# Kernel optimization log

Hardware: AMD Instinct MI355X
Metric: run time of the kernel (lower is better)

The kernel has to match this reference:

```python
import jax, jax.numpy as jnp
import numpy as np

B, T, HID = 2, 2048, 2048
NH, NKV, D = 16, 4, 128
WIN = 512
ROPE_BASE = 10000.0
SCALE = D ** -0.5
EPS = 1e-12


def setup_inputs() -> dict:
    key = jax.random.key(0)
    ks = jax.random.split(key, 5)
    x = jax.random.normal(ks[0], (B, T, HID), dtype=jnp.float32)
    wq = jax.random.normal(ks[1], (HID, NH * D), dtype=jnp.float32) * 0.02
    wk = jax.random.normal(ks[2], (HID, NKV * D), dtype=jnp.float32) * 0.02
    wv = jax.random.normal(ks[3], (HID, NKV * D), dtype=jnp.float32) * 0.02
    wo = jax.random.normal(ks[4], (NH * D, HID), dtype=jnp.float32) * 0.02
    return {"x": x, "wq": wq, "wk": wk, "wv": wv, "wo": wo}


def _rope_tables(t, offset=0):
    inv_freq = 1.0 / (ROPE_BASE ** (jnp.arange(0, D, 2, dtype=jnp.float32) / D))
    pos = jnp.arange(offset, offset + t, dtype=jnp.float32)
    freqs = pos[:, None] * inv_freq[None, :]              # [t, D/2]
    cos = jnp.concatenate([jnp.cos(freqs), jnp.cos(freqs)], axis=-1)  # [t, D]
    sin = jnp.concatenate([jnp.sin(freqs), jnp.sin(freqs)], axis=-1)
    return cos, sin


def _apply_rope(x, cos, sin):
    # x: [B, H, T, D]; rotate-half formulation
    x1, x2 = jnp.split(x, 2, axis=-1)
    rot = jnp.concatenate([-x2, x1], axis=-1)
    return x * cos[None, None] + rot * sin[None, None]


def _l2norm(x):
    n = jnp.sqrt(jnp.sum(x * x, axis=-1, keepdims=True))
    return x / jnp.maximum(n, EPS)


def _forward(x, wq, wk, wv, wo):
    b, t, _ = x.shape
    q = (x @ wq).reshape(b, t, NH, D).transpose(0, 2, 1, 3)    # [B,H,T,D]
    k = (x @ wk).reshape(b, t, NKV, D).transpose(0, 2, 1, 3)   # [B,Hk,T,D]
    v = (x @ wv).reshape(b, t, NKV, D).transpose(0, 2, 1, 3)
    q = _l2norm(q)
    k = _l2norm(k)
    cos, sin = _rope_tables(t, offset=0)
    q = _apply_rope(q, cos, sin)
    k = _apply_rope(k, cos, sin)
    rep = NH // NKV
    k = jnp.repeat(k, rep, axis=1)                             # GQA repeat_interleave
    v = jnp.repeat(v, rep, axis=1)
    i = jnp.arange(t)
    allowed = (i[None, :] <= i[:, None]) & (i[None, :] > i[:, None] - WIN)  # [T,T]
    logits = jnp.einsum("bhid,bhjd->bhij", q, k) * SCALE
    logits = jnp.where(allowed[None, None], logits, -jnp.inf)
    attn = jax.nn.softmax(logits, axis=-1)
    out = jnp.einsum("bhij,bhjd->bhid", attn, v)
    out = out.transpose(0, 2, 1, 3).reshape(b, t, NH * D)
    return out @ wo


def reference(x, wq, wk, wv, wo):
    return _forward(x, wq, wk, wv, wo)
```

## Files before the change

kernel.cpp:

```cpp
#include <hip/hip_runtime.h>
#include <hip/hip_bf16.h>
#include <cstdint>

#define NHQ 16
#define NKVH 4
#define HDIM 128
#define WINSZ 512
#define TSEQ 2048
#define ATTN_SCALE 0.08838834764831845f

typedef __attribute__((ext_vector_type(8))) short s16x8;
typedef __attribute__((ext_vector_type(4))) float f32x4;

__device__ __forceinline__ void gload16(const void* g, void* lds) {
  __builtin_amdgcn_global_load_lds(
      (const __attribute__((address_space(1))) unsigned int*)g,
      (__attribute__((address_space(3))) unsigned int*)(uintptr_t)lds,
      16, 0, 0);
}

__device__ __forceinline__ f32x4 mfma16(s16x8 a, s16x8 b, f32x4 c) {
  return __builtin_amdgcn_mfma_f32_16x16x32_bf16(a, b, c, 0, 0, 0);
}

#define SBAR() asm volatile("s_barrier" ::: "memory")
#define VMCNT(n) asm volatile("s_waitcnt vmcnt(" #n ")" ::: "memory")
#define LGKM(n) asm volatile("s_waitcnt lgkmcnt(" #n ")" ::: "memory")

__global__ __launch_bounds__(256) void rope_tables_kernel(float* __restrict__ cosT,
                                                          float* __restrict__ sinT) {
  int idx = blockIdx.x * 256 + threadIdx.x;
  int t = idx >> 6, d2 = idx & 63;
  float inv = powf(10000.0f, -(float)d2 / 64.0f);
  float a = (float)t * inv;
  cosT[idx] = cosf(a);
  sinT[idx] = sinf(a);
}

__global__ __launch_bounds__(256) void cast_kernel(const float* __restrict__ in,
                                                   __bf16* __restrict__ out, int n4) {
  int i = blockIdx.x * 256 + threadIdx.x;
  if (i >= n4) return;
  float4 v = ((const float4*)in)[i];
  union { __bf16 h[4]; uint2 u; } pk;
  pk.h[0] = (__bf16)v.x; pk.h[1] = (__bf16)v.y; pk.h[2] = (__bf16)v.z; pk.h[3] = (__bf16)v.w;
  ((uint2*)out)[i] = pk.u;
}

__global__ __launch_bounds__(256) void transpose_cast(const float* __restrict__ in,
                                                      __bf16* __restrict__ out, int R, int C) {
  __shared__ float tile[32][33];
  int c0 = blockIdx.x * 32, r0 = blockIdx.y * 32;
  int tx = threadIdx.x, ty = threadIdx.y;
#pragma unroll
  for (int i = 0; i < 4; i++)
    tile[ty + i * 8][tx] = in[(size_t)(r0 + ty + i * 8) * C + c0 + tx];
  __syncthreads();
#pragma unroll
  for (int i = 0; i < 4; i++)
    out[(size_t)(c0 + ty + i * 8) * R + r0 + tx] = (__bf16)tile[tx][ty + i * 8];
}

template <int MODE>
__global__ __launch_bounds__(512, 2) void gemm8(const __bf16* __restrict__ A,
                                                const __bf16* __restrict__ Bt,
                                                float* __restrict__ Cf,
                                                __bf16* __restrict__ Qo, __bf16* __restrict__ Ko,
                                                __bf16* __restrict__ Vo, int M, int N, int K) {
  __shared__ __attribute__((aligned(16))) char Lds[2][65536];

  const int tid = threadIdx.x;
  const int w = tid >> 6, lane = tid & 63;
  const int wm = w >> 2, wn = w & 3;

  const int nbx = gridDim.x;
  const int nwg = nbx * gridDim.y;
  const int bid = blockIdx.y * nbx + blockIdx.x;
  const int q8 = nwg >> 3, r8 = nwg & 7;
  const int xcd = bid & 7, idx = bid >> 3;
  const int swz = (xcd < r8 ? xcd * (q8 + 1) : r8 * (q8 + 1) + (xcd - r8) * q8) + idx;
  const int bx = swz % nbx, by = swz / nbx;
  const int m0 = by * 256, n0 = bx * 256;

  const int ru = tid >> 3;
  const int cs = (tid & 7) ^ (ru & 7);
  const __bf16* gAs = A + (size_t)(m0 + ru) * K + cs * 8;
  const __bf16* gBs = Bt + (size_t)(n0 + ru) * K + cs * 8;

  auto stA = [&](int tt, int u) {
    gload16(gAs + (size_t)(64 * u) * K + tt * 64, Lds[tt & 1] + u * 8192 + w * 1024);
  };
  auto stB = [&](int tt, int u) {
    gload16(gBs + (size_t)(64 * u) * K + tt * 64, Lds[tt & 1] + 32768 + u * 8192 + w * 1024);
  };

  const int rowb = (lane & 15) * 128;
  const int cph0 = (((lane >> 4)) ^ (lane & 7)) * 16;
  const int cph1 = ((4 + (lane >> 4)) ^ (lane & 7)) * 16;
  const int Abase = wm * 16384;
  const int Bbase = 32768 + wn * 8192;

  f32x4 acc[8][4];
  f32x4 zero = {0.f, 0.f, 0.f, 0.f};
#pragma unroll
  for (int i = 0; i < 8; i++)
#pragma unroll
    for (int j = 0; j < 4; j++) acc[i][j] = zero;

  const int NT = K >> 6;

#pragma unroll
  for (int u = 0; u < 4; u++) stA(0, u);
#pragma unroll
  for (int u = 0; u < 4; u++) stB(0, u);
#pragma unroll
  for (int u = 0; u < 4; u++) stA(1, u);
#pragma unroll
  for (int u = 0; u < 4; u++) stB(1, u);
  VMCNT(8);
  SBAR();

  s16x8 fa[4][2], fb[4][2];

  for (int t = 0; t < NT; ++t) {
    const char* bs = Lds[t & 1];
    const bool more = (t + 2) < NT;

#pragma unroll
    for (int mi = 0; mi < 4; mi++) {
      fa[mi][0] = *(const s16x8*)(bs + Abase + mi * 2048 + rowb + cph0);
      fa[mi][1] = *(const s16x8*)(bs + Abase + mi * 2048 + rowb + cph1);
    }
#pragma unroll
    for (int ni = 0; ni < 2; ni++) {
      fb[ni][0] = *(const s16x8*)(bs + Bbase + ni * 2048 + rowb + cph0);
      fb[ni][1] = *(const s16x8*)(bs + Bbase + ni * 2048 + rowb + cph1);
    }
    SBAR();
    LGKM(0);
    __builtin_amdgcn_sched_barrier(0);
    __builtin_amdgcn_s_setprio(1);
#pragma unroll
    for (int mi = 0; mi < 4; mi++)
#pragma unroll
      for (int ni = 0; ni < 2; ni++)
#pragma unroll
        for (int kk = 0; kk < 2; kk++)
          acc[mi][ni] = mfma16(fa[mi][kk], fb[ni][kk], acc[mi][ni]);
    __builtin_amdgcn_s_setprio(0);
    SBAR();

#pragma unroll
    for (int ni = 2; ni < 4; ni++) {
      fb[ni][0] = *(const s16x8*)(bs + Bbase + ni * 2048 + rowb + cph0);
      fb[ni][1] = *(const s16x8*)(bs + Bbase + ni * 2048 + rowb + cph1);
    }
    if (more) { stA(t + 2, 0); stA(t + 2, 2); }
    SBAR();
    LGKM(0);
    __builtin_amdgcn_sched_barrier(0);
    __builtin_amdgcn_s_setprio(1);
#pragma unroll
    for (int mi = 0; mi < 4; mi++)
#pragma unroll
      for (int ni = 2; ni < 4; ni++)
#pragma unroll
        for (int kk = 0; kk < 2; kk++)
          acc[mi][ni] = mfma16(fa[mi][kk], fb[ni][kk], acc[mi][ni]);
    __builtin_amdgcn_s_setprio(0);
    SBAR();

#pragma unroll
    for (int mi = 0; mi < 4; mi++) {
      fa[mi][0] = *(const s16x8*)(bs + Abase + 8192 + mi * 2048 + rowb + cph0);
      fa[mi][1] = *(const s16x8*)(bs + Abase + 8192 + mi * 2048 + rowb + cph1);
    }
    if (more) { stB(t + 2, 0); stB(t + 2, 1); stB(t + 2, 2); stB(t + 2, 3); }
    SBAR();
    LGKM(0);
    __builtin_amdgcn_sched_barrier(0);
    __builtin_amdgcn_s_setprio(1);
#pragma unroll
    for (int mi = 0; mi < 4; mi++)
#pragma unroll
      for (int ni = 0; ni < 2; ni++)
#pragma unroll
        for (int kk = 0; kk < 2; kk++)
          acc[4 + mi][ni] = mfma16(fa[mi][kk], fb[ni][kk], acc[4 + mi][ni]);
    __builtin_amdgcn_s_setprio(0);
    SBAR();

    if (more) { stA(t + 2, 1); stA(t + 2, 3); }
    if (t + 2 < NT) {
      VMCNT(8);
    } else if (t + 1 < NT) {
      VMCNT(0);
    }
    SBAR();
    __builtin_amdgcn_s_setprio(1);
#pragma unroll
    for (int mi = 0; mi < 4; mi++)
#pragma unroll
      for (int ni = 2; ni < 4; ni++)
#pragma unroll
        for (int kk = 0; kk < 2; kk++)
          acc[4 + mi][ni] = mfma16(fa[mi][kk], fb[ni][kk], acc[4 + mi][ni]);
    __builtin_amdgcn_s_setprio(0);
    SBAR();
  }

#pragma unroll
  for (int mf = 0; mf < 8; mf++)
#pragma unroll
    for (int nf = 0; nf < 4; nf++) {
      int rbase = m0 + wm * 128 + mf * 16 + (lane >> 4) * 4;
      int col = n0 + wn * 64 + nf * 16 + (lane & 15);
#pragma unroll
      for (int r = 0; r < 4; r++) {
        int m = rbase + r;
        float v = acc[mf][nf][r];
        if constexpr (MODE == 0) {
          Cf[(size_t)m * N + col] = v;
        } else {
          int b = m >> 11, tq = m & 2047;
          __bf16 bv = (__bf16)v;
          if (col < 2048) {
            Qo[(((size_t)(b * NHQ + (col >> 7))) * TSEQ + tq) * HDIM + (col & 127)] = bv;
          } else if (col < 2560) {
            int c2 = col - 2048;
            Ko[(((size_t)(b * NKVH + (c2 >> 7))) * TSEQ + tq) * HDIM + (c2 & 127)] = bv;
          } else {
            int c2 = col - 2560;
            Vo[(((size_t)(b * NKVH + (c2 >> 7))) * TSEQ + tq) * HDIM + (c2 & 127)] = bv;
          }
        }
      }
    }
}

__global__ __launch_bounds__(256) void normrope(__bf16* __restrict__ Q, __bf16* __restrict__ Kk,
                                                const float* __restrict__ cosT,
                                                const float* __restrict__ sinT) {
  int w = threadIdx.x >> 6, lane = threadIdx.x & 63;
  int row = blockIdx.x / 5;
  int slot = (blockIdx.x % 5) * 4 + w;
  int b = row >> 11, t = row & 2047;
  __bf16* p;
  if (slot < 16)
    p = Q + (((size_t)(b * NHQ + slot)) * TSEQ + t) * HDIM;
  else
    p = Kk + (((size_t)(b * NKVH + (slot - 16))) * TSEQ + t) * HDIM;
  float x1 = (float)p[lane], x2 = (float)p[lane + 64];
  float ss = x1 * x1 + x2 * x2;
#pragma unroll
  for (int off = 32; off; off >>= 1) ss += __shfl_xor(ss, off);
  float inv = 1.0f / fmaxf(sqrtf(ss), 1e-12f);
  x1 *= inv;
  x2 *= inv;
  float c = cosT[t * 64 + lane], s = sinT[t * 64 + lane];
  p[lane] = (__bf16)(x1 * c - x2 * s);
  p[lane + 64] = (__bf16)(x2 * c + x1 * s);
}

__global__ __launch_bounds__(256) void attn_kernel(const __bf16* __restrict__ Qf,
                                                   const __bf16* __restrict__ Kf,
                                                   const __bf16* __restrict__ Vf,
                                                   __bf16* __restrict__ Ab) {
  __shared__ __align__(16) __bf16 Kl[32 * 136];
  __shared__ __align__(16) __bf16 Vt[128 * 40];
  __shared__ __align__(16) __bf16 Pl[4][16 * 40];
  int tid = threadIdx.x, w = tid >> 6, lane = tid & 63;
  int bid = blockIdx.x;
  int qt = bid & 31, h = (bid >> 5) & 15, b = bid >> 9;
  int qs = qt * 64;
  int kvh = h >> 2;
  const __bf16* Qb = Qf + ((size_t)(b * NHQ + h) * TSEQ) * HDIM;
  const __bf16* Kb = Kf + ((size_t)(b * NKVH + kvh) * TSEQ) * HDIM;
  const __bf16* Vb = Vf + ((size_t)(b * NKVH + kvh) * TSEQ) * HDIM;

  s16x8 aq[4];
  int qrow_f = qs + w * 16 + (lane & 15);
#pragma unroll
  for (int kb = 0; kb < 4; kb++)
    aq[kb] = *(const s16x8*)(Qb + (size_t)qrow_f * HDIM + kb * 32 + (lane >> 4) * 8);

  f32x4 acc[8];
  f32x4 zero = {0.f, 0.f, 0.f, 0.f};
#pragma unroll
  for (int db = 0; db < 8; db++) acc[db] = zero;
  float mrow[4], lrow[4];
#pragma unroll
  for (int r = 0; r < 4; r++) { mrow[r] = -1e30f; lrow[r] = 0.f; }

  int lo = qs - (WINSZ - 1);
  if (lo < 0) lo = 0;
  lo &= ~31;

  for (int ks = lo; ks <= qs + 63; ks += 32) {
    __syncthreads();
#pragma unroll
    for (int i = 0; i < 2; i++) {
      int c = tid + 256 * i;
      int j = c >> 4, dk = (c & 15) * 8;
      int4 kv = *(const int4*)(Kb + (size_t)(ks + j) * HDIM + dk);
      *(int4*)&Kl[j * 136 + dk] = kv;
      int jv = c & 31, d0 = (c >> 5) * 8;
      int4 vv = *(const int4*)(Vb + (size_t)(ks + jv) * HDIM + d0);
      const __bf16* pv = (const __bf16*)&vv;
#pragma unroll
      for (int e = 0; e < 8; e++) Vt[(d0 + e) * 40 + jv] = pv[e];
    }
    __syncthreads();

    f32x4 sacc[2];
    sacc[0] = zero; sacc[1] = zero;
#pragma unroll
    for (int jb = 0; jb < 2; jb++)
#pragma unroll
      for (int kb = 0; kb < 4; kb++) {
        s16x8 bk = *(const s16x8*)&Kl[(jb * 16 + (lane & 15)) * 136 + kb * 32 + (lane >> 4) * 8];
        sacc[jb] = mfma16(aq[kb], bk, sacc[jb]);
      }

    int colbase = ks + (lane & 15);
    float p0v[4], p1v[4], scf[4];
#pragma unroll
    for (int r = 0; r < 4; r++) {
      int qrow = qs + w * 16 + (lane >> 4) * 4 + r;
      float s0 = sacc[0][r] * ATTN_SCALE, s1 = sacc[1][r] * ATTN_SCALE;
      int j0 = colbase, j1 = colbase + 16;
      bool a0 = (j0 <= qrow) && (j0 > qrow - WINSZ);
      bool a1 = (j1 <= qrow) && (j1 > qrow - WINSZ);
      float mt = fmaxf(a0 ? s0 : -1e30f, a1 ? s1 : -1e30f);
#pragma unroll
      for (int off = 1; off < 16; off <<= 1) mt = fmaxf(mt, __shfl_xor(mt, off));
      float mn = fmaxf(mrow[r], mt);
      float p0 = a0 ? __expf(s0 - mn) : 0.f;
      float p1 = a1 ? __expf(s1 - mn) : 0.f;
      float sf = __expf(mrow[r] - mn);
      float ts = p0 + p1;
#pragma unroll
      for (int off = 1; off < 16; off <<= 1) ts += __shfl_xor(ts, off);
      lrow[r] = lrow[r] * sf + ts;
      mrow[r] = mn;
      p0v[r] = p0; p1v[r] = p1; scf[r] = sf;
    }

#pragma unroll
    for (int r = 0; r < 4; r++) {
      Pl[w][((lane >> 4) * 4 + r) * 40 + 0 * 16 + (lane & 15)] = (__bf16)p0v[r];
      Pl[w][((lane >> 4) * 4 + r) * 40 + 1 * 16 + (lane & 15)] = (__bf16)p1v[r];
    }
#pragma unroll
    for (int db = 0; db < 8; db++) {
      f32x4 t = acc[db];
#pragma unroll
      for (int r = 0; r < 4; r++) t[r] *= scf[r];
      acc[db] = t;
    }

    s16x8 pa = *(const s16x8*)&Pl[w][(lane & 15) * 40 + (lane >> 4) * 8];
#pragma unroll
    for (int db = 0; db < 8; db++) {
      s16x8 bv = *(const s16x8*)&Vt[(db * 16 + (lane & 15)) * 40 + (lane >> 4) * 8];
      acc[db] = mfma16(pa, bv, acc[db]);
    }
  }

#pragma unroll
  for (int db = 0; db < 8; db++)
#pragma unroll
    for (int r = 0; r < 4; r++) {
      int qrow = qs + w * 16 + (lane >> 4) * 4 + r;
      float v = acc[db][r] / lrow[r];
      Ab[((size_t)(b * TSEQ + qrow)) * 2048 + h * HDIM + db * 16 + (lane & 15)] = (__bf16)v;
    }
}

extern "C" void kernel_launch(void* const* d_in, const int* in_sizes, int n_in,
                              void* d_out, int out_size, void* d_ws, size_t ws_size,
                              hipStream_t stream) {
  const float* x = (const float*)d_in[0];
  const float* wq = (const float*)d_in[1];
  const float* wk = (const float*)d_in[2];
  const float* wv = (const float*)d_in[3];
  const float* wo = (const float*)d_in[4];
  float* out = (float*)d_out;

  char* ws = (char*)d_ws;
  size_t off = 0;
  auto alloc = [&](size_t bytes) -> void* {
    void* p = ws + off;
    off += (bytes + 255) & ~(size_t)255;
    return p;
  };
  __bf16* Xb = (__bf16*)alloc((size_t)4096 * 2048 * 2);
  __bf16* Wqkvt = (__bf16*)alloc((size_t)3072 * 2048 * 2);
  __bf16* Wot = (__bf16*)alloc((size_t)2048 * 2048 * 2);
  __bf16* Q = (__bf16*)alloc((size_t)2 * NHQ * TSEQ * HDIM * 2);
  __bf16* Kb = (__bf16*)alloc((size_t)2 * NKVH * TSEQ * HDIM * 2);
  __bf16* Vb = (__bf16*)alloc((size_t)2 * NKVH * TSEQ * HDIM * 2);
  float* cosT = (float*)alloc((size_t)TSEQ * 64 * 4);
  float* sinT = (float*)alloc((size_t)TSEQ * 64 * 4);
  __bf16* Ab = Xb;

  rope_tables_kernel<<<TSEQ * 64 / 256, 256, 0, stream>>>(cosT, sinT);
  cast_kernel<<<8192, 256, 0, stream>>>(x, Xb, 2097152);
  dim3 tb(32, 8);
  transpose_cast<<<dim3(64, 64), tb, 0, stream>>>(wq, Wqkvt, 2048, 2048);
  transpose_cast<<<dim3(16, 64), tb, 0, stream>>>(wk, Wqkvt + (size_t)2048 * 2048, 2048, 512);
  transpose_cast<<<dim3(16, 64), tb, 0, stream>>>(wv, Wqkvt + (size_t)2560 * 2048, 2048, 512);
  transpose_cast<<<dim3(64, 64), tb, 0, stream>>>(wo, Wot, 2048, 2048);

  gemm8<1><<<dim3(12, 16), 512, 0, stream>>>(Xb, Wqkvt, nullptr, Q, Kb, Vb, 4096, 3072, 2048);
  normrope<<<4096 * 5, 256, 0, stream>>>(Q, Kb, cosT, sinT);
  attn_kernel<<<2 * NHQ * (TSEQ / 64), 256, 0, stream>>>(Q, Kb, Vb, Ab);
  gemm8<0><<<dim3(8, 16), 512, 0, stream>>>(Ab, Wot, out, nullptr, nullptr, nullptr, 4096, 2048,
                                            2048);
}
```

Measured before the change: 233.2 us.

## Pre-transpose V and software-pipeline attention with 64-key tiles and swizzled LDS

```diff
diff --git a/kernel.cpp b/kernel.cpp
--- a/kernel.cpp
+++ b/kernel.cpp
@@ -59,6 +59,23 @@
 #pragma unroll
   for (int i = 0; i < 4; i++)
     out[(size_t)(c0 + ty + i * 8) * R + r0 + tx] = (__bf16)tile[tx][ty + i * 8];
+}
+
+__global__ __launch_bounds__(256) void vtrans(const __bf16* __restrict__ V,
+                                              __bf16* __restrict__ VT) {
+  __shared__ __bf16 t32[32][33];
+  int bh = blockIdx.z;
+  int t0 = blockIdx.y * 32, d0 = blockIdx.x * 32;
+  const __bf16* src = V + (size_t)bh * TSEQ * HDIM;
+  __bf16* dst = VT + (size_t)bh * HDIM * TSEQ;
+  int tx = threadIdx.x, ty = threadIdx.y;
+#pragma unroll
+  for (int i = 0; i < 4; i++)
+    t32[ty + i * 8][tx] = src[(size_t)(t0 + ty + i * 8) * HDIM + d0 + tx];
+  __syncthreads();
+#pragma unroll
+  for (int i = 0; i < 4; i++)
+    dst[(size_t)(d0 + ty + i * 8) * TSEQ + t0 + tx] = t32[tx][ty + i * 8];
 }
 
 template <int MODE>
@@ -264,11 +281,11 @@
 
 __global__ __launch_bounds__(256) void attn_kernel(const __bf16* __restrict__ Qf,
                                                    const __bf16* __restrict__ Kf,
-                                                   const __bf16* __restrict__ Vf,
+                                                   const __bf16* __restrict__ VTf,
                                                    __bf16* __restrict__ Ab) {
-  __shared__ __align__(16) __bf16 Kl[32 * 136];
-  __shared__ __align__(16) __bf16 Vt[128 * 40];
-  __shared__ __align__(16) __bf16 Pl[4][16 * 40];
+  __shared__ __attribute__((aligned(16))) char KlB[64 * 256];
+  __shared__ __attribute__((aligned(16))) char VtB[128 * 128];
+  __shared__ __attribute__((aligned(16))) char PlB[4 * 2048];
   int tid = threadIdx.x, w = tid >> 6, lane = tid & 63;
   int bid = blockIdx.x;
   int qt = bid & 31, h = (bid >> 5) & 15, b = bid >> 9;
@@ -276,7 +293,8 @@
   int kvh = h >> 2;
   const __bf16* Qb = Qf + ((size_t)(b * NHQ + h) * TSEQ) * HDIM;
   const __bf16* Kb = Kf + ((size_t)(b * NKVH + kvh) * TSEQ) * HDIM;
-  const __bf16* Vb = Vf + ((size_t)(b * NKVH + kvh) * TSEQ) * HDIM;
+  const __bf16* VTb = VTf + ((size_t)(b * NKVH + kvh) * HDIM) * TSEQ;
+  char* Pw = PlB + w * 2048;
 
   s16x8 aq[4];
   int qrow_f = qs + w * 16 + (lane & 15);
@@ -294,78 +312,117 @@
 
   int lo = qs - (WINSZ - 1);
   if (lo < 0) lo = 0;
-  lo &= ~31;
-
-  for (int ks = lo; ks <= qs + 63; ks += 32) {
+  lo &= ~63;
+  const int nt = ((qs + 64) - lo) >> 6;
+
+  int4 kE[4], vE[4], kO[4], vO[4];
+
+#define ATTN_LOAD(KR, VR, KS)                                                      \
+  _Pragma("unroll") for (int i = 0; i < 4; i++) {                                  \
+    KR[i] = *(const int4*)(Kb + (size_t)((KS) + (tid >> 4) + 16 * i) * HDIM +      \
+                           (tid & 15) * 8);                                        \
+    VR[i] = *(const int4*)(VTb + (size_t)((tid >> 3) + 32 * i) * TSEQ + (KS) +     \
+                           (tid & 7) * 8);                                         \
+  }
+
+#define ATTN_WRITE(KR, VR)                                                         \
+  _Pragma("unroll") for (int i = 0; i < 4; i++) {                                  \
+    int jrow = (tid >> 4) + 16 * i;                                                \
+    *(int4*)(KlB + jrow * 256 + (((tid & 15) * 16) ^ ((jrow & 7) << 4))) = KR[i];  \
+    int drow = (tid >> 3) + 32 * i;                                                \
+    *(int4*)(VtB + drow * 128 + (((tid & 7) * 16) ^ ((drow & 7) << 4))) = VR[i];   \
+  }
+
+#define ATTN_COMPUTE(KS)                                                           \
+  {                                                                                \
+    f32x4 sacc[4];                                                                 \
+    _Pragma("unroll") for (int jb = 0; jb < 4; jb++) sacc[jb] = zero;              \
+    _Pragma("unroll") for (int jb = 0; jb < 4; jb++) {                             \
+      int key = jb * 16 + (lane & 15);                                             \
+      _Pragma("unroll") for (int kb = 0; kb < 4; kb++) {                           \
+        s16x8 bk = *(const s16x8*)(KlB + key * 256 +                               \
+                                   ((kb * 64 + (lane >> 4) * 16) ^ ((key & 7) << 4))); \
+        sacc[jb] = mfma16(aq[kb], bk, sacc[jb]);                                   \
+      }                                                                            \
+    }                                                                              \
+    float scf[4];                                                                  \
+    _Pragma("unroll") for (int r = 0; r < 4; r++) {                                \
+      int qrow = qs + w * 16 + (lane >> 4) * 4 + r;                                \
+      float sv[4]; bool av[4];                                                     \
+      _Pragma("unroll") for (int jb = 0; jb < 4; jb++) {                           \
+        int j = (KS) + jb * 16 + (lane & 15);                                      \
+        av[jb] = (j <= qrow) && (j > qrow - WINSZ);                                \
+        sv[jb] = sacc[jb][r] * ATTN_SCALE;                                         \
+      }                                                                            \
+      float mt = -1e30f;                                                           \
+      _Pragma("unroll") for (int jb = 0; jb < 4; jb++)                             \
+        mt = fmaxf(mt, av[jb] ? sv[jb] : -1e30f);                                  \
+      _Pragma("unroll") for (int off = 1; off < 16; off <<= 1)                     \
+        mt = fmaxf(mt, __shfl_xor(mt, off));                                       \
+      float mn = fmaxf(mrow[r], mt);                                               \
+      float pv_[4]; float ts = 0.f;                                                \
+      _Pragma("unroll") for (int jb = 0; jb < 4; jb++) {                           \
+        pv_[jb] = av[jb] ? __expf(sv[jb] - mn) : 0.f;                              \
+        ts += pv_[jb];                                                             \
+      }                                                                            \
+      _Pragma("unroll") for (int off = 1; off < 16; off <<= 1)                     \
+        ts += __shfl_xor(ts, off);                                                 \
+      float sf = __expf(mrow[r] - mn);                                             \
+      lrow[r] = lrow[r] * sf + ts;                                                 \
+      mrow[r] = mn;                                                                \
+      scf[r] = sf;                                                                 \
+      int q = (lane >> 4) * 4 + r;                                                 \
+      _Pragma("unroll") for (int jb = 0; jb < 4; jb++)                             \
+        *(__bf16*)(Pw + q * 128 +                                                  \
+                   (((jb * 16 + (lane & 15)) * 2) ^ ((q & 7) << 4))) = (__bf16)pv_[jb]; \
+    }                                                                              \
+    _Pragma("unroll") for (int db = 0; db < 8; db++) {                             \
+      f32x4 tt = acc[db];                                                          \
+      _Pragma("unroll") for (int r = 0; r < 4; r++) tt[r] *= scf[r];               \
+      acc[db] = tt;                                                                \
+    }                                                                              \
+    s16x8 pa[2];                                                                   \
+    _Pragma("unroll") for (int kb = 0; kb < 2; kb++) {                             \
+      int q = lane & 15;                                                           \
+      pa[kb] = *(const s16x8*)(Pw + q * 128 +                                      \
+                               ((kb * 64 + (lane >> 4) * 16) ^ ((q & 7) << 4)));   \
+    }                                                                              \
+    _Pragma("unroll") for (int db = 0; db < 8; db++) {                             \
+      int d = db * 16 + (lane & 15);                                               \
+      _Pragma("unroll") for (int kb = 0; kb < 2; kb++) {                           \
+        s16x8 bv = *(const s16x8*)(VtB + d * 128 +                                 \
+                                   ((kb * 64 + (lane >> 4) * 16) ^ ((d & 7) << 4))); \
+        acc[db] = mfma16(pa[kb], bv, acc[db]);                                     \
+      }                                                                            \
+    }                                                                              \
+  }
+
+  int ks = lo;
+  ATTN_LOAD(kE, vE, ks);
+  int it = 0;
+  for (; it + 2 <= nt; it += 2) {
+    ATTN_WRITE(kE, vE);
+    ATTN_LOAD(kO, vO, ks + 64);
     __syncthreads();
-#pragma unroll
-    for (int i = 0; i < 2; i++) {
-      int c = tid + 256 * i;
-      int j = c >> 4, dk = (c & 15) * 8;
-      int4 kv = *(const int4*)(Kb + (size_t)(ks + j) * HDIM + dk);
-      *(int4*)&Kl[j * 136 + dk] = kv;
-      int jv = c & 31, d0 = (c >> 5) * 8;
-      int4 vv = *(const int4*)(Vb + (size_t)(ks + jv) * HDIM + d0);
-      const __bf16* pv = (const __bf16*)&vv;
-#pragma unroll
-      for (int e = 0; e < 8; e++) Vt[(d0 + e) * 40 + jv] = pv[e];
-    }
+    ATTN_COMPUTE(ks);
     __syncthreads();
-
-    f32x4 sacc[2];
-    sacc[0] = zero; sacc[1] = zero;
-#pragma unroll
-    for (int jb = 0; jb < 2; jb++)
-#pragma unroll
-      for (int kb = 0; kb < 4; kb++) {
-        s16x8 bk = *(const s16x8*)&Kl[(jb * 16 + (lane & 15)) * 136 + kb * 32 + (lane >> 4) * 8];
-        sacc[jb] = mfma16(aq[kb], bk, sacc[jb]);
-      }
-
-    int colbase = ks + (lane & 15);
-    float p0v[4], p1v[4], scf[4];
-#pragma unroll
-    for (int r = 0; r < 4; r++) {
-      int qrow = qs + w * 16 + (lane >> 4) * 4 + r;
-      float s0 = sacc[0][r] * ATTN_SCALE, s1 = sacc[1][r] * ATTN_SCALE;
-      int j0 = colbase, j1 = colbase + 16;
-      bool a0 = (j0 <= qrow) && (j0 > qrow - WINSZ);
-      bool a1 = (j1 <= qrow) && (j1 > qrow - WINSZ);
-      float mt = fmaxf(a0 ? s0 : -1e30f, a1 ? s1 : -1e30f);
-#pragma unroll
-      for (int off = 1; off < 16; off <<= 1) mt = fmaxf(mt, __shfl_xor(mt, off));
-      float mn = fmaxf(mrow[r], mt);
-      float p0 = a0 ? __expf(s0 - mn) : 0.f;
-      float p1 = a1 ? __expf(s1 - mn) : 0.f;
-      float sf = __expf(mrow[r] - mn);
-      float ts = p0 + p1;
-#pragma unroll
-      for (int off = 1; off < 16; off <<= 1) ts += __shfl_xor(ts, off);
-      lrow[r] = lrow[r] * sf + ts;
-      mrow[r] = mn;
-      p0v[r] = p0; p1v[r] = p1; scf[r] = sf;
-    }
-
-#pragma unroll
-    for (int r = 0; r < 4; r++) {
-      Pl[w][((lane >> 4) * 4 + r) * 40 + 0 * 16 + (lane & 15)] = (__bf16)p0v[r];
-      Pl[w][((lane >> 4) * 4 + r) * 40 + 1 * 16 + (lane & 15)] = (__bf16)p1v[r];
-    }
-#pragma unroll
-    for (int db = 0; db < 8; db++) {
-      f32x4 t = acc[db];
-#pragma unroll
-      for (int r = 0; r < 4; r++) t[r] *= scf[r];
-      acc[db] = t;
-    }
-
-    s16x8 pa = *(const s16x8*)&Pl[w][(lane & 15) * 40 + (lane >> 4) * 8];
-#pragma unroll
-    for (int db = 0; db < 8; db++) {
-      s16x8 bv = *(const s16x8*)&Vt[(db * 16 + (lane & 15)) * 40 + (lane >> 4) * 8];
-      acc[db] = mfma16(pa, bv, acc[db]);
-    }
-  }
+    ks += 64;
+    ATTN_WRITE(kO, vO);
+    if (it + 2 < nt) ATTN_LOAD(kE, vE, ks + 64);
+    __syncthreads();
+    ATTN_COMPUTE(ks);
+    __syncthreads();
+    ks += 64;
+  }
+  if (it < nt) {
+    ATTN_WRITE(kE, vE);
+    __syncthreads();
+    ATTN_COMPUTE(ks);
+  }
+
+#undef ATTN_LOAD
+#undef ATTN_WRITE
+#undef ATTN_COMPUTE
 
 #pragma unroll
   for (int db = 0; db < 8; db++)
@@ -403,6 +460,7 @@
   float* cosT = (float*)alloc((size_t)TSEQ * 64 * 4);
   float* sinT = (float*)alloc((size_t)TSEQ * 64 * 4);
   __bf16* Ab = Xb;
+  __bf16* VT = Wqkvt;
 
   rope_tables_kernel<<<TSEQ * 64 / 256, 256, 0, stream>>>(cosT, sinT);
   cast_kernel<<<8192, 256, 0, stream>>>(x, Xb, 2097152);
@@ -413,8 +471,9 @@
   transpose_cast<<<dim3(64, 64), tb, 0, stream>>>(wo, Wot, 2048, 2048);
 
   gemm8<1><<<dim3(12, 16), 512, 0, stream>>>(Xb, Wqkvt, nullptr, Q, Kb, Vb, 4096, 3072, 2048);
+  vtrans<<<dim3(4, 64, 2 * NKVH), tb, 0, stream>>>(Vb, VT);
   normrope<<<4096 * 5, 256, 0, stream>>>(Q, Kb, cosT, sinT);
-  attn_kernel<<<2 * NHQ * (TSEQ / 64), 256, 0, stream>>>(Q, Kb, Vb, Ab);
+  attn_kernel<<<2 * NHQ * (TSEQ / 64), 256, 0, stream>>>(Q, Kb, VT, Ab);
   gemm8<0><<<dim3(8, 16), 512, 0, stream>>>(Ab, Wot, out, nullptr, nullptr, nullptr, 4096, 2048,
                                             2048);
 }
```

Result: slower. 271.9 us (+16.6%).
